# Performance work log

Hardware: AMD Instinct MI355X
Metric: run time of the kernel (lower is better)

## Reference

```python
import jax, jax.numpy as jnp
import numpy as np

DT = 1.0
EPS = 1e-6


def setup_inputs() -> dict:
    key = jax.random.key(0)
    ks = jax.random.split(key, 5)
    B, I, H = 8192, 512, 1024
    scale = (6.0 / ((1 + 5.0) * (I + H))) ** 0.5  # kaiming_uniform with a=sqrt(5) bound
    return {
        "x": jax.random.normal(ks[0], (B, I), dtype=jnp.float32),
        "hidden": jax.random.normal(ks[1], (B, H), dtype=jnp.float32),
        "W_tau": jax.random.uniform(ks[2], (H, I + H), dtype=jnp.float32, minval=-scale, maxval=scale),
        "b_tau": jnp.zeros((H,), dtype=jnp.float32),
        "W_r": jax.random.uniform(ks[3], (H, I + H), dtype=jnp.float32, minval=-scale, maxval=scale),
        "b_r": jnp.zeros((H,), dtype=jnp.float32),
        "W_h": jax.random.uniform(ks[4], (H, I + H), dtype=jnp.float32, minval=-scale, maxval=scale),
        "b_h": jnp.zeros((H,), dtype=jnp.float32),
    }


def reference(x, hidden, W_tau, b_tau, W_r, b_r, W_h, b_h):
    combined = jnp.concatenate([x, hidden], axis=1)          # [B, I+H]
    tau = jax.nn.softplus(combined @ W_tau.T + b_tau) + EPS  # [B, H]
    r = jax.nn.sigmoid(combined @ W_r.T + b_r)               # [B, H]
    gated = r * hidden
    cand_in = jnp.concatenate([x, gated], axis=1)            # [B, I+H]
    h_tilde = jnp.tanh(cand_in @ W_h.T + b_h)                # [B, H]
    return hidden + DT * (h_tilde - hidden) / tau
```

## Files before the change

### kernel.cpp

```cpp
#include <hip/hip_runtime.h>
#include <hip/hip_bf16.h>

typedef __attribute__((ext_vector_type(8))) unsigned short u16x8;
typedef __attribute__((ext_vector_type(8))) __bf16        bf16x8;
typedef __attribute__((ext_vector_type(4))) float         f32x4;

static constexpr int B_ = 8192;
static constexpr int I_ = 512;
static constexpr int H_ = 1024;
static constexpr int K_ = 1536;
static constexpr int NT    = K_ / 64;
static constexpr int NITER = NT / 2;

#define AS1 __attribute__((address_space(1)))
#define AS3 __attribute__((address_space(3)))

__device__ __forceinline__ unsigned short f2bf(float f) {
    unsigned int u = __float_as_uint(f);
    u += 0x7FFF + ((u >> 16) & 1);
    return (unsigned short)(u >> 16);
}
__device__ __forceinline__ float bf2f(unsigned short u) {
    return __uint_as_float(((unsigned int)u) << 16);
}

__device__ __forceinline__ void memfence() { asm volatile("" ::: "memory"); }
__device__ __forceinline__ void barrier_() {
    memfence(); __builtin_amdgcn_s_barrier(); memfence();
}
__device__ __forceinline__ void vwait4() {
    asm volatile("s_waitcnt vmcnt(4)" ::: "memory");
    __builtin_amdgcn_sched_barrier(0);
}

__device__ __forceinline__ u16x8 cvt8(const float4* s) {
    float4 a = s[0], b = s[1];
    u16x8 o;
    o[0] = f2bf(a.x); o[1] = f2bf(a.y); o[2] = f2bf(a.z); o[3] = f2bf(a.w);
    o[4] = f2bf(b.x); o[5] = f2bf(b.y); o[6] = f2bf(b.z); o[7] = f2bf(b.w);
    return o;
}

__global__ void prep(const float* __restrict__ x, const float* __restrict__ hid,
                     const float* __restrict__ wt, const float* __restrict__ wr,
                     const float* __restrict__ wh,
                     unsigned short* __restrict__ cmb1,
                     unsigned short* __restrict__ wtb,
                     unsigned short* __restrict__ wrb,
                     unsigned short* __restrict__ whb) {
    constexpr int NX8 = B_ * I_ / 8;
    constexpr int NH8 = B_ * H_ / 8;
    constexpr int NW8 = H_ * K_ / 8;
    int i = blockIdx.x * blockDim.x + threadIdx.x;
    if (i < NX8) {
        int row = i >> 6, c8 = i & 63;
        u16x8 o = cvt8((const float4*)x + (size_t)i * 2);
        *(u16x8*)(cmb1 + (size_t)row * K_ + c8 * 8) = o;
    } else if (i < NX8 + NH8) {
        int j = i - NX8;
        int row = j >> 7, c8 = j & 127;
        u16x8 o = cvt8((const float4*)hid + (size_t)j * 2);
        *(u16x8*)(cmb1 + (size_t)row * K_ + 512 + c8 * 8) = o;
    } else {
        int k = i - (NX8 + NH8);
        const float* src; unsigned short* dst;
        if (k < NW8)          { src = wt; dst = wtb; }
        else if (k < 2 * NW8) { src = wr; dst = wrb; k -= NW8; }
        else                  { src = wh; dst = whb; k -= 2 * NW8; }
        u16x8 o = cvt8((const float4*)src + (size_t)k * 2);
        *(u16x8*)(dst + (size_t)k * 8) = o;
    }
}

template<int MODE>
__global__ __launch_bounds__(512, 1)
void gemm4(const unsigned short* __restrict__ A1,
           const unsigned short* __restrict__ A2,
           const unsigned short* __restrict__ W0,
           const float* __restrict__ bias0,
           const unsigned short* __restrict__ itau_in,
           float* __restrict__ outF,
           unsigned short* __restrict__ itau_out,
           unsigned short* __restrict__ gate_out)
{
    extern __shared__ __align__(16) char lds[];

    const int t = threadIdx.x;
    const int w = t >> 6, l = t & 63;
    const int wg  = blockIdx.y * 8 + blockIdx.x;
    const int swz = (wg & 7) * 32 + (wg >> 3);
    const int m0  = (swz >> 3) * 256;
    const int n0  = (swz & 7) * 128;

    const int srow  = t >> 3;
    const int sslot = ((t & 7) ^ (srow & 7)) * 8;
    const unsigned short* srcA1 = A1 + (size_t)(m0 + srow) * K_ + sslot;
    const unsigned short* srcA2 = A2 + (size_t)(m0 + srow) * K_ + sslot;
    const unsigned short* srcB  = W0 + (size_t)(n0 + srow) * K_ + sslot;
    char* dstA = lds + w * 1024;
    char* dstB = lds + 65536 + w * 1024;

    auto stageA = [&](int tt, int h) {
        const unsigned short* base = (MODE == 2 && tt >= 8) ? srcA2 : srcA1;
        const unsigned short* s = base + (size_t)(h * 128) * K_ + tt * 64;
        char* d = dstA + (tt & 1) * 32768 + h * 16384;
        #pragma unroll
        for (int j = 0; j < 2; ++j)
            __builtin_amdgcn_global_load_lds(
                (const AS1 void*)(s + (size_t)j * 64 * K_),
                (AS3 void*)(d + j * 8192), 16, 0, 0);
    };
    auto stageB = [&](int tt, int h) {
        const unsigned short* s = srcB + (size_t)(h * 64) * K_ + tt * 64;
        char* d = dstB + (tt & 1) * 16384 + h * 8192;
        __builtin_amdgcn_global_load_lds((const AS1 void*)s, (AS3 void*)d, 16, 0, 0);
    };

    const int fr = l & 15, kq = l >> 4;
    const int wm = w >> 1, wn = w & 1;
    const int fx = (kq ^ (fr & 7)) << 4;
    const char* rdA0 = lds + (wm * 32 + fr) * 128 + fx;
    const char* rdA1 = lds + (wm * 32 + fr) * 128 + (fx ^ 64);
    const char* rdB0 = lds + 65536 + (wn * 32 + fr) * 128 + fx;
    const char* rdB1 = lds + 65536 + (wn * 32 + fr) * 128 + (fx ^ 64);

    bf16x8 af[2][2], bfr[2][2][2];
    f32x4 acc[4][4];
    #pragma unroll
    for (int i = 0; i < 4; ++i)
        #pragma unroll
        for (int jn = 0; jn < 4; ++jn) acc[i][jn] = (f32x4)0.0f;

    auto readA = [&](int half, int par) {
        #pragma unroll
        for (int mi = 0; mi < 2; ++mi) {
            af[mi][0] = *(const bf16x8*)(rdA0 + par * 32768 + half * 16384 + mi * 2048);
            af[mi][1] = *(const bf16x8*)(rdA1 + par * 32768 + half * 16384 + mi * 2048);
        }
    };
    auto readBall = [&](int par) {
        #pragma unroll
        for (int bh = 0; bh < 2; ++bh)
            #pragma unroll
            for (int ni = 0; ni < 2; ++ni) {
                bfr[bh][ni][0] = *(const bf16x8*)(rdB0 + par * 16384 + bh * 8192 + ni * 2048);
                bfr[bh][ni][1] = *(const bf16x8*)(rdB1 + par * 16384 + bh * 8192 + ni * 2048);
            }
    };
    auto quad16 = [&](int ah) {
        __builtin_amdgcn_s_setprio(1);
        #pragma unroll
        for (int bh = 0; bh < 2; ++bh)
            #pragma unroll
            for (int mi = 0; mi < 2; ++mi)
                #pragma unroll
                for (int ni = 0; ni < 2; ++ni)
                    #pragma unroll
                    for (int ks = 0; ks < 2; ++ks)
                        acc[ah * 2 + mi][bh * 2 + ni] =
                            __builtin_amdgcn_mfma_f32_16x16x32_bf16(
                                af[mi][ks], bfr[bh][ni][ks],
                                acc[ah * 2 + mi][bh * 2 + ni], 0, 0, 0);
        __builtin_amdgcn_s_setprio(0);
    };

    stageA(0, 0); stageA(0, 1); stageB(0, 0); stageB(0, 1);
    stageA(1, 0); stageB(1, 0); stageB(1, 1);
    vwait4(); barrier_();

    for (int j = 0; j < NITER; ++j) {
        const int tE = (2 * j + 2 < NT) ? 2 * j + 2 : 0;
        const int tO = (2 * j + 3 < NT) ? 2 * j + 3 : 0;
        readA(0, 0); readBall(0); stageA(2 * j + 1, 1);
        quad16(0); barrier_();
        readA(1, 0); stageA(tE, 0); stageB(tE, 0); stageB(tE, 1);
        quad16(1); vwait4(); barrier_();
        readA(0, 1); readBall(1); stageA(tE, 1);
        quad16(0); barrier_();
        readA(1, 1); stageA(tO, 0); stageB(tO, 0); stageB(tO, 1);
        quad16(1); vwait4(); barrier_();
    }
    asm volatile("s_waitcnt vmcnt(0)" ::: "memory");

    const int rs4 = kq * 4;
    const int nB0 = n0 + wn * 32;
    const int mB0 = m0 + wm * 32;
    #pragma unroll
    for (int ah = 0; ah < 2; ++ah)
        #pragma unroll
        for (int mi = 0; mi < 2; ++mi)
            #pragma unroll
            for (int bh = 0; bh < 2; ++bh)
                #pragma unroll
                for (int ni = 0; ni < 2; ++ni) {
                    const int n = nB0 + bh * 64 + ni * 16 + fr;
                    const float bv = bias0[n];
                    #pragma unroll
                    for (int jj = 0; jj < 4; ++jj) {
                        const int m = mB0 + ah * 128 + mi * 16 + rs4 + jj;
                        const size_t ix = (size_t)m * H_ + n;
                        const size_t hx = (size_t)m * K_ + 512 + n;
                        const float z = acc[ah * 2 + mi][bh * 2 + ni][jj] + bv;
                        if (MODE == 0) {
                            const float sp = (z > 15.f) ? z : __logf(1.0f + __expf(z));
                            itau_out[ix] = f2bf(__fdividef(1.0f, sp + 1e-6f));
                        } else if (MODE == 1) {
                            const float r = __fdividef(1.0f, 1.0f + __expf(-z));
                            gate_out[hx] = f2bf(r * bf2f(A1[hx]));
                        } else {
                            const float e2 = __expf(2.0f * z);
                            const float th = __fdividef(e2 - 1.0f, e2 + 1.0f);
                            const float h = bf2f(A1[hx]);
                            const float it = bf2f(itau_in[ix]);
                            outF[ix] = h + (th - h) * it;
                        }
                    }
                }
}

extern "C" void kernel_launch(void* const* d_in, const int* in_sizes, int n_in,
                              void* d_out, int out_size, void* d_ws, size_t ws_size,
                              hipStream_t stream) {
    (void)in_sizes; (void)n_in; (void)out_size; (void)ws_size;

    const float* x     = (const float*)d_in[0];
    const float* hid   = (const float*)d_in[1];
    const float* W_tau = (const float*)d_in[2];
    const float* b_tau = (const float*)d_in[3];
    const float* W_r   = (const float*)d_in[4];
    const float* b_r   = (const float*)d_in[5];
    const float* W_h   = (const float*)d_in[6];
    const float* b_h   = (const float*)d_in[7];

    unsigned short* cmb1 = (unsigned short*)d_ws;
    unsigned short* cmb2 = cmb1 + (size_t)B_ * K_;
    unsigned short* wtb  = cmb2 + (size_t)B_ * K_;
    unsigned short* wrb  = wtb  + (size_t)H_ * K_;
    unsigned short* whb  = wrb  + (size_t)H_ * K_;
    unsigned short* itau = whb  + (size_t)H_ * K_;

    hipFuncSetAttribute(reinterpret_cast<const void*>(&gemm4<0>),
                        hipFuncAttributeMaxDynamicSharedMemorySize, 98304);
    hipFuncSetAttribute(reinterpret_cast<const void*>(&gemm4<1>),
                        hipFuncAttributeMaxDynamicSharedMemorySize, 98304);
    hipFuncSetAttribute(reinterpret_cast<const void*>(&gemm4<2>),
                        hipFuncAttributeMaxDynamicSharedMemorySize, 98304);

    const int th = 256;
    constexpr int NPREP = B_ * I_ / 8 + B_ * H_ / 8 + 3 * H_ * K_ / 8;
    prep<<<NPREP / th, th, 0, stream>>>(x, hid, W_tau, W_r, W_h,
                                        cmb1, wtb, wrb, whb);

    dim3 g(8, 32);
    gemm4<0><<<g, 512, 98304, stream>>>(cmb1, cmb1, wtb, b_tau, nullptr,
                                        nullptr, itau, nullptr);
    gemm4<1><<<g, 512, 98304, stream>>>(cmb1, cmb1, wrb, b_r, nullptr,
                                        nullptr, nullptr, cmb2);
    gemm4<2><<<g, 512, 98304, stream>>>(cmb1, cmb2, whb, b_h, itau,
                                        (float*)d_out, nullptr, nullptr);
}
```

Measured before the change: 109.8 us.

## Load B fragments directly to registers, bypassing LDS, and read fp32 hidden in epilogue

The weight (B) operand is no longer staged through LDS. Each wave now loads its MFMA B fragments straight from global memory into two register sets that are double-buffered across K tiles. Only the A tile is staged via LDS, which cuts LDS to 64KB and removes the B LDS reads, with the pipeline and wait counts restructured to match. The epilogue reads the fp32 hidden input instead of the bf16 copy, which changes precision slightly. This trades LDS traffic for more uncoalesced global loads and higher register pressure, and each wave re-reads the weights from global/L2.

Measured after the change: 218.8 us. 99.2% more time.

```diff
diff --git a/kernel.cpp b/kernel.cpp
--- a/kernel.cpp
+++ b/kernel.cpp
@@ -9,8 +9,7 @@
 static constexpr int I_ = 512;
 static constexpr int H_ = 1024;
 static constexpr int K_ = 1536;
-static constexpr int NT    = K_ / 64;
-static constexpr int NITER = NT / 2;
+static constexpr int NT = K_ / 64;
 
 #define AS1 __attribute__((address_space(1)))
 #define AS3 __attribute__((address_space(3)))
@@ -28,10 +27,15 @@
 __device__ __forceinline__ void barrier_() {
     memfence(); __builtin_amdgcn_s_barrier(); memfence();
 }
-__device__ __forceinline__ void vwait4() {
-    asm volatile("s_waitcnt vmcnt(4)" ::: "memory");
+__device__ __forceinline__ void vwait8() {
+    asm volatile("s_waitcnt vmcnt(8)" ::: "memory");
     __builtin_amdgcn_sched_barrier(0);
 }
+__device__ __forceinline__ void vwait12() {
+    asm volatile("s_waitcnt vmcnt(12)" ::: "memory");
+    __builtin_amdgcn_sched_barrier(0);
+}
+__device__ __forceinline__ void schedpin() { __builtin_amdgcn_sched_barrier(0); }
 
 __device__ __forceinline__ u16x8 cvt8(const float4* s) {
     float4 a = s[0], b = s[1];
@@ -74,10 +78,11 @@
 
 template<int MODE>
 __global__ __launch_bounds__(512, 1)
-void gemm4(const unsigned short* __restrict__ A1,
+void gemmL(const unsigned short* __restrict__ A1,
            const unsigned short* __restrict__ A2,
            const unsigned short* __restrict__ W0,
            const float* __restrict__ bias0,
+           const float* __restrict__ hidden,
            const unsigned short* __restrict__ itau_in,
            float* __restrict__ outF,
            unsigned short* __restrict__ itau_out,
@@ -96,24 +101,17 @@
     const int sslot = ((t & 7) ^ (srow & 7)) * 8;
     const unsigned short* srcA1 = A1 + (size_t)(m0 + srow) * K_ + sslot;
     const unsigned short* srcA2 = A2 + (size_t)(m0 + srow) * K_ + sslot;
-    const unsigned short* srcB  = W0 + (size_t)(n0 + srow) * K_ + sslot;
     char* dstA = lds + w * 1024;
-    char* dstB = lds + 65536 + w * 1024;
-
-    auto stageA = [&](int tt, int h) {
+
+    auto stageA = [&](int tt) {
         const unsigned short* base = (MODE == 2 && tt >= 8) ? srcA2 : srcA1;
-        const unsigned short* s = base + (size_t)(h * 128) * K_ + tt * 64;
-        char* d = dstA + (tt & 1) * 32768 + h * 16384;
-        #pragma unroll
-        for (int j = 0; j < 2; ++j)
+        const unsigned short* s = base + tt * 64;
+        char* d = dstA + (tt & 1) * 32768;
+        #pragma unroll
+        for (int q = 0; q < 4; ++q)
             __builtin_amdgcn_global_load_lds(
-                (const AS1 void*)(s + (size_t)j * 64 * K_),
-                (AS3 void*)(d + j * 8192), 16, 0, 0);
-    };
-    auto stageB = [&](int tt, int h) {
-        const unsigned short* s = srcB + (size_t)(h * 64) * K_ + tt * 64;
-        char* d = dstB + (tt & 1) * 16384 + h * 8192;
-        __builtin_amdgcn_global_load_lds((const AS1 void*)s, (AS3 void*)d, 16, 0, 0);
+                (const AS1 void*)(s + (size_t)q * 64 * K_),
+                (AS3 void*)(d + q * 8192), 16, 0, 0);
     };
 
     const int fr = l & 15, kq = l >> 4;
@@ -121,10 +119,11 @@
     const int fx = (kq ^ (fr & 7)) << 4;
     const char* rdA0 = lds + (wm * 32 + fr) * 128 + fx;
     const char* rdA1 = lds + (wm * 32 + fr) * 128 + (fx ^ 64);
-    const char* rdB0 = lds + 65536 + (wn * 32 + fr) * 128 + fx;
-    const char* rdB1 = lds + 65536 + (wn * 32 + fr) * 128 + (fx ^ 64);
-
-    bf16x8 af[2][2], bfr[2][2][2];
+
+    const unsigned short* baseB = W0 + (size_t)(n0 + wn * 32 + fr) * K_ + kq * 8;
+
+    bf16x8 af[2][2];
+    bf16x8 BA[2][2][2], BB[2][2][2];
     f32x4 acc[4][4];
     #pragma unroll
     for (int i = 0; i < 4; ++i)
@@ -138,16 +137,18 @@
             af[mi][1] = *(const bf16x8*)(rdA1 + par * 32768 + half * 16384 + mi * 2048);
         }
     };
-    auto readBall = [&](int par) {
+    auto loadB = [&](bf16x8 (&Bq)[2][2][2], int tt) {
+        const unsigned short* p = baseB + tt * 64;
         #pragma unroll
         for (int bh = 0; bh < 2; ++bh)
             #pragma unroll
-            for (int ni = 0; ni < 2; ++ni) {
-                bfr[bh][ni][0] = *(const bf16x8*)(rdB0 + par * 16384 + bh * 8192 + ni * 2048);
-                bfr[bh][ni][1] = *(const bf16x8*)(rdB1 + par * 16384 + bh * 8192 + ni * 2048);
-            }
-    };
-    auto quad16 = [&](int ah) {
+            for (int ni = 0; ni < 2; ++ni)
+                #pragma unroll
+                for (int ks = 0; ks < 2; ++ks)
+                    Bq[bh][ni][ks] = *(const bf16x8*)(p
+                        + (size_t)(bh * 64 + ni * 16) * K_ + ks * 32);
+    };
+    auto quad16 = [&](const bf16x8 (&Bq)[2][2][2], int ah) {
         __builtin_amdgcn_s_setprio(1);
         #pragma unroll
         for (int bh = 0; bh < 2; ++bh)
@@ -159,27 +160,30 @@
                     for (int ks = 0; ks < 2; ++ks)
                         acc[ah * 2 + mi][bh * 2 + ni] =
                             __builtin_amdgcn_mfma_f32_16x16x32_bf16(
-                                af[mi][ks], bfr[bh][ni][ks],
+                                af[mi][ks], Bq[bh][ni][ks],
                                 acc[ah * 2 + mi][bh * 2 + ni], 0, 0, 0);
         __builtin_amdgcn_s_setprio(0);
     };
 
-    stageA(0, 0); stageA(0, 1); stageB(0, 0); stageB(0, 1);
-    stageA(1, 0); stageB(1, 0); stageB(1, 1);
-    vwait4(); barrier_();
-
-    for (int j = 0; j < NITER; ++j) {
-        const int tE = (2 * j + 2 < NT) ? 2 * j + 2 : 0;
-        const int tO = (2 * j + 3 < NT) ? 2 * j + 3 : 0;
-        readA(0, 0); readBall(0); stageA(2 * j + 1, 1);
-        quad16(0); barrier_();
-        readA(1, 0); stageA(tE, 0); stageB(tE, 0); stageB(tE, 1);
-        quad16(1); vwait4(); barrier_();
-        readA(0, 1); readBall(1); stageA(tE, 1);
-        quad16(0); barrier_();
-        readA(1, 1); stageA(tO, 0); stageB(tO, 0); stageB(tO, 1);
-        quad16(1); vwait4(); barrier_();
+    stageA(0); schedpin(); loadB(BA, 0); schedpin();
+    stageA(1); schedpin(); loadB(BB, 1); schedpin();
+    vwait12(); barrier_();
+
+    #define CLMP(X) (((X) < NT) ? (X) : 0)
+    for (int j = 0; j < NT / 2; ++j) {
+        const int te = 2 * j, to = 2 * j + 1;
+        readA(0, 0); quad16(BA, 0);
+        readA(1, 0); quad16(BA, 1);
+        vwait8(); barrier_();
+        stageA(CLMP(te + 2)); schedpin(); loadB(BA, CLMP(te + 2)); schedpin();
+        vwait12();
+        readA(0, 1); quad16(BB, 0);
+        readA(1, 1); quad16(BB, 1);
+        vwait8(); barrier_();
+        stageA(CLMP(to + 2)); schedpin(); loadB(BB, CLMP(to + 2)); schedpin();
+        vwait12();
     }
+    #undef CLMP
     asm volatile("s_waitcnt vmcnt(0)" ::: "memory");
 
     const int rs4 = kq * 4;
@@ -199,18 +203,17 @@
                     for (int jj = 0; jj < 4; ++jj) {
                         const int m = mB0 + ah * 128 + mi * 16 + rs4 + jj;
                         const size_t ix = (size_t)m * H_ + n;
-                        const size_t hx = (size_t)m * K_ + 512 + n;
                         const float z = acc[ah * 2 + mi][bh * 2 + ni][jj] + bv;
                         if (MODE == 0) {
                             const float sp = (z > 15.f) ? z : __logf(1.0f + __expf(z));
                             itau_out[ix] = f2bf(__fdividef(1.0f, sp + 1e-6f));
                         } else if (MODE == 1) {
                             const float r = __fdividef(1.0f, 1.0f + __expf(-z));
-                            gate_out[hx] = f2bf(r * bf2f(A1[hx]));
+                            gate_out[(size_t)m * K_ + 512 + n] = f2bf(r * hidden[ix]);
                         } else {
                             const float e2 = __expf(2.0f * z);
                             const float th = __fdividef(e2 - 1.0f, e2 + 1.0f);
-                            const float h = bf2f(A1[hx]);
+                            const float h = hidden[ix];
                             const float it = bf2f(itau_in[ix]);
                             outF[ix] = h + (th - h) * it;
                         }
@@ -239,12 +242,12 @@
     unsigned short* whb  = wrb  + (size_t)H_ * K_;
     unsigned short* itau = whb  + (size_t)H_ * K_;
 
-    hipFuncSetAttribute(reinterpret_cast<const void*>(&gemm4<0>),
-                        hipFuncAttributeMaxDynamicSharedMemorySize, 98304);
-    hipFuncSetAttribute(reinterpret_cast<const void*>(&gemm4<1>),
-                        hipFuncAttributeMaxDynamicSharedMemorySize, 98304);
-    hipFuncSetAttribute(reinterpret_cast<const void*>(&gemm4<2>),
-                        hipFuncAttributeMaxDynamicSharedMemorySize, 98304);
+    hipFuncSetAttribute(reinterpret_cast<const void*>(&gemmL<0>),
+                        hipFuncAttributeMaxDynamicSharedMemorySize, 65536);
+    hipFuncSetAttribute(reinterpret_cast<const void*>(&gemmL<1>),
+                        hipFuncAttributeMaxDynamicSharedMemorySize, 65536);
+    hipFuncSetAttribute(reinterpret_cast<const void*>(&gemmL<2>),
+                        hipFuncAttributeMaxDynamicSharedMemorySize, 65536);
 
     const int th = 256;
     constexpr int NPREP = B_ * I_ / 8 + B_ * H_ / 8 + 3 * H_ * K_ / 8;
@@ -252,10 +255,10 @@
                                         cmb1, wtb, wrb, whb);
 
     dim3 g(8, 32);
-    gemm4<0><<<g, 512, 98304, stream>>>(cmb1, cmb1, wtb, b_tau, nullptr,
+    gemmL<0><<<g, 512, 65536, stream>>>(cmb1, cmb1, wtb, b_tau, hid, nullptr,
                                         nullptr, itau, nullptr);
-    gemm4<1><<<g, 512, 98304, stream>>>(cmb1, cmb1, wrb, b_r, nullptr,
+    gemmL<1><<<g, 512, 65536, stream>>>(cmb1, cmb1, wrb, b_r, hid, nullptr,
                                         nullptr, nullptr, cmb2);
-    gemm4<2><<<g, 512, 98304, stream>>>(cmb1, cmb2, whb, b_h, itau,
+    gemmL<2><<<g, 512, 65536, stream>>>(cmb1, cmb2, whb, b_h, hid, itau,
                                         (float*)d_out, nullptr, nullptr);
 }
```
